# Kernel optimization log

Hardware: AMD Instinct MI355X
Metric: run time of the kernel (lower is better)

The kernel has to match this reference:

```python
import jax, jax.numpy as jnp
import numpy as np

N_EMBD = 384
HEAD_SIZE = 16

def setup_inputs() -> dict:
    key = jax.random.key(0)
    k1, k2, k3, k4 = jax.random.split(key, 4)
    B, T = 4, 4096
    x = jax.random.normal(k1, (B, T, N_EMBD), dtype=jnp.float32)
    # nn.Linear(n_embd, head_size, bias=False): y = x @ W^T, W: [head_size, n_embd].
    # Store transposed [n_embd, head_size] for direct matmul.
    s = 1.0 / np.sqrt(N_EMBD)
    Wk = jax.random.uniform(k2, (N_EMBD, HEAD_SIZE), jnp.float32, -s, s)
    Wq = jax.random.uniform(k3, (N_EMBD, HEAD_SIZE), jnp.float32, -s, s)
    Wv = jax.random.uniform(k4, (N_EMBD, HEAD_SIZE), jnp.float32, -s, s)
    return {"x": x, "Wk": Wk, "Wq": Wq, "Wv": Wv}

def reference(x, Wk, Wq, Wv):
    B, T, C = x.shape
    k = x @ Wk  # [B,T,H]
    q = x @ Wq
    v = x @ Wv
    scale = k.shape[-1] ** -0.5
    wei = jnp.einsum('bth,bsh->bts', q, k) * scale  # [B,T,T]
    causal = jnp.tril(jnp.ones((T, T), dtype=bool))
    wei = jnp.where(causal, wei, -jnp.inf)
    wei = jax.nn.softmax(wei, axis=-1)
    out = jnp.einsum('bts,bsh->bth', wei, v)  # [B,T,H]
    return out
```

## Files before the change

### kernel.cpp

```cpp
#include <hip/hip_runtime.h>


constexpr int B_DIM = 4;
constexpr int T_SEQ = 4096;
constexpr int C_DIM = 384;
constexpr int H_DIM = 16;
constexpr int NROW  = B_DIM * T_SEQ;

constexpr int WTROW = 392;
constexpr int WTMAT = 16 * WTROW;

typedef __bf16 bf16x8 __attribute__((ext_vector_type(8)));
typedef float  f32x4  __attribute__((ext_vector_type(4)));

__device__ __forceinline__ unsigned short f2bf(float f) {
  unsigned int u = __builtin_bit_cast(unsigned int, f);
  u += 0x7fffu + ((u >> 16) & 1u);
  return (unsigned short)(u >> 16);
}
__device__ __forceinline__ bf16x8 as_bf16x8(uint4 u) {
  return __builtin_bit_cast(bf16x8, u);
}
__device__ __forceinline__ unsigned cvt_pk_bf16(float lo, float hi) {
  unsigned r;
  asm("v_cvt_pk_bf16_f32 %0, %1, %2" : "=v"(r) : "v"(lo), "v"(hi));
  return r;
}

__global__ __launch_bounds__(512) void qkvw(
    const float* __restrict__ x,  const float* __restrict__ Wk,
    const float* __restrict__ Wq, const float* __restrict__ Wv,
    unsigned short* __restrict__ Kb,
    unsigned short* __restrict__ Qb,
    unsigned short* __restrict__ VTb)
{
  __shared__ __attribute__((aligned(16))) unsigned short WTl[3 * WTMAT];
  __shared__ float mrg[4][12 * 64];

  const int tid  = threadIdx.x;
  const int w    = tid >> 6;
  const int lane = tid & 63;
  const int quad = lane >> 4;
  const int col  = lane & 15;
  const int pair = w >> 1;
  const int kw   = w & 1;
  const int tile = (blockIdx.x << 2) | pair;
  const int r0   = tile << 4;
  const int kb   = kw * 6;

  {
    const float* const Ws[3] = {Wk, Wq, Wv};
#pragma unroll
    for (int e = 0; e < 9; ++e) {
      const int i4 = e * 512 + tid;
      const int m  = i4 / 1536;
      const int j4 = (i4 - m * 1536) * 4;
      const int k  = j4 >> 4;
      const int n  = j4 & 15;
      const float4 v = *reinterpret_cast<const float4*>(Ws[m] + j4);
      unsigned short* const dst = WTl + m * WTMAT + k;
      dst[(n + 0) * WTROW] = f2bf(v.x);
      dst[(n + 1) * WTROW] = f2bf(v.y);
      dst[(n + 2) * WTROW] = f2bf(v.z);
      dst[(n + 3) * WTROW] = f2bf(v.w);
    }
  }
  __syncthreads();

  const float4* __restrict__ xp =
      reinterpret_cast<const float4*>(x + (size_t)(r0 + col) * C_DIM) + quad * 2;
  float4 araw[12];
#pragma unroll
  for (int kk = 0; kk < 6; ++kk) {
    araw[2 * kk]     = xp[(kb + kk) * 8];
    araw[2 * kk + 1] = xp[(kb + kk) * 8 + 1];
  }

  const unsigned short* const bkl = WTl + col * WTROW + quad * 8;

  f32x4 ck = {0.f, 0.f, 0.f, 0.f};
  f32x4 cq = {0.f, 0.f, 0.f, 0.f};
  f32x4 cv = {0.f, 0.f, 0.f, 0.f};
#pragma unroll
  for (int kk = 0; kk < 6; ++kk) {
    uint4 pk;
    const float4 a0 = araw[2 * kk], a1 = araw[2 * kk + 1];
    pk.x = cvt_pk_bf16(a0.x, a0.y);
    pk.y = cvt_pk_bf16(a0.z, a0.w);
    pk.z = cvt_pk_bf16(a1.x, a1.y);
    pk.w = cvt_pk_bf16(a1.z, a1.w);
    const bf16x8 av = as_bf16x8(pk);
    const int ko = (kb + kk) * 32;
    const uint4 fk = *reinterpret_cast<const uint4*>(bkl + ko);
    const uint4 fq = *reinterpret_cast<const uint4*>(bkl + WTMAT + ko);
    const uint4 fv = *reinterpret_cast<const uint4*>(bkl + 2 * WTMAT + ko);
    ck = __builtin_amdgcn_mfma_f32_16x16x32_bf16(av, as_bf16x8(fk), ck, 0, 0, 0);
    cq = __builtin_amdgcn_mfma_f32_16x16x32_bf16(av, as_bf16x8(fq), cq, 0, 0, 0);
    cv = __builtin_amdgcn_mfma_f32_16x16x32_bf16(av, as_bf16x8(fv), cv, 0, 0, 0);
  }

  if (kw == 1) {
#pragma unroll
    for (int r = 0; r < 4; ++r) {
      mrg[pair][r * 64 + lane]       = ck[r];
      mrg[pair][(4 + r) * 64 + lane] = cq[r];
      mrg[pair][(8 + r) * 64 + lane] = cv[r];
    }
  }
  __syncthreads();
  if (kw == 0) {
    const float SC = 0.25f * 1.44269504088896341f;
#pragma unroll
    for (int r = 0; r < 4; ++r) {
      const float vk = ck[r] + mrg[pair][r * 64 + lane];
      const float vq = cq[r] + mrg[pair][(4 + r) * 64 + lane];
      const float vv = cv[r] + mrg[pair][(8 + r) * 64 + lane];
      const int row = r0 + quad * 4 + r;
      Kb[row * 16 + col]      = f2bf(vk);
      Qb[row * 32 + col]      = f2bf(vq * SC);
      Qb[row * 32 + 16 + col] = 0;
      const int bb = row >> 12, t = row & 4095;
      VTb[(((size_t)(bb * 16 + col)) << 12) + t] = f2bf(vv);
    }
  }
}

__global__ __launch_bounds__(512) void flash_v9(
    const unsigned short* __restrict__ Qb,
    const unsigned short* __restrict__ Kb,
    const unsigned short* __restrict__ VTb,
    float* __restrict__ out)
{
  const int tid  = threadIdx.x;
  const int w    = tid >> 6;
  const int lane = tid & 63;
  const int quad = lane >> 4;
  const int col  = lane & 15;
  const int p    = blockIdx.x >> 2;
  const int b    = blockIdx.x & 3;
  const int qtA  = 255 - p;
  const int qtB  = p;
  const int nchA = (qtA + 4) >> 2;

  __shared__ __attribute__((aligned(16))) unsigned short Pl[8][16 * 72];
  __shared__ float mO[8][2][256];
  __shared__ float mL[8][2][16];
  unsigned short* const P = Pl[w];

  const unsigned short* Kbase = Kb + ((size_t)(b * T_SEQ) << 4);
  const unsigned short* Vbase = VTb + (((size_t)(b * 16 + col)) << 12);
  const int poff = col * 72 + quad * 4;

  f32x4 o = {0.f, 0.f, 0.f, 0.f};

  const uint4* qpA = reinterpret_cast<const uint4*>(
      Qb + (((size_t)(b * T_SEQ + (qtA << 4) + col)) << 5) + quad * 8);
  const uint4* qpB = reinterpret_cast<const uint4*>(
      Qb + (((size_t)(b * T_SEQ + (qtB << 4) + col)) << 5) + quad * 8);
  const bf16x8 qaA = as_bf16x8(qpA[0]);
  const bf16x8 qaB = as_bf16x8(qpB[0]);

  auto loadK = [&](int c, uint4* k4) {
    const int kt0 = c << 2;
#pragma unroll
    for (int t = 0; t < 4; ++t)
      k4[t] = *reinterpret_cast<const uint4*>(
          Kbase + (((size_t)((kt0 + t) * 16 + col)) << 4) + quad * 8);
  };
  auto loadV = [&](int c, uint4* v2) {
    v2[0] = *reinterpret_cast<const uint4*>(Vbase + c * 64 + quad * 8);
    v2[1] = *reinterpret_cast<const uint4*>(Vbase + c * 64 + 32 + quad * 8);
  };

  auto computeP = [&](int qt, bf16x8 qa, int c, const uint4* k4, float& lref) {
    const int kt0 = c << 2;
    float lsum = 0.f;
#pragma unroll
    for (int t = 0; t < 4; ++t) {
      const int kt = kt0 + t;
      f32x4 sf;
      if (kt <= qt) {
        f32x4 z = {0.f, 0.f, 0.f, 0.f};
        sf = __builtin_amdgcn_mfma_f32_16x16x32_bf16(as_bf16x8(k4[t]), qa, z, 0, 0, 0);
        if (kt == qt) {
#pragma unroll
          for (int r = 0; r < 4; ++r)
            if (quad * 4 + r > col) sf[r] = -1e30f;
        }
      } else {
#pragma unroll
        for (int r = 0; r < 4; ++r) sf[r] = -1e30f;
      }
      const float p0 = __builtin_amdgcn_exp2f(sf[0]);
      const float p1 = __builtin_amdgcn_exp2f(sf[1]);
      const float p2 = __builtin_amdgcn_exp2f(sf[2]);
      const float p3 = __builtin_amdgcn_exp2f(sf[3]);
      lsum += (p0 + p1) + (p2 + p3);
      uint2 pr;
      pr.x = cvt_pk_bf16(p0, p1);
      pr.y = cvt_pk_bf16(p2, p3);
      *reinterpret_cast<uint2*>(P + poff + t * 16) = pr;
    }
    lref += lsum;
  };

  auto doPV = [&](const uint4* v2) {
    const uint2* pp = reinterpret_cast<const uint2*>(P + col * 72);
    const uint2 a0 = pp[quad * 2],     a1 = pp[quad * 2 + 1];
    const uint2 b0 = pp[8 + quad * 2], b1 = pp[8 + quad * 2 + 1];
    const uint4 p0 = {a0.x, a0.y, a1.x, a1.y};
    const uint4 p1 = {b0.x, b0.y, b1.x, b1.y};
    o = __builtin_amdgcn_mfma_f32_16x16x32_bf16(as_bf16x8(p0), as_bf16x8(v2[0]), o, 0, 0, 0);
    o = __builtin_amdgcn_mfma_f32_16x16x32_bf16(as_bf16x8(p1), as_bf16x8(v2[1]), o, 0, 0, 0);
  };

  auto writePartial = [&](int ph, float lsum) {
    float l = lsum;
    l += __shfl_xor(l, 16);
    l += __shfl_xor(l, 32);
#pragma unroll
    for (int r = 0; r < 4; ++r)
      mO[w][ph][(quad * 4 + r) * 16 + col] = o[r];
    if (quad == 0) mL[w][ph][col] = l;
  };

  float lA = 0.f, lB = 0.f;
  uint4 k4[4], vcur[2], vnxt[2];

  int g = w;
  loadK(g, k4);
  loadV(g, vcur);
  computeP(qtA, qaA, g, k4, lA);

  int prevg = g;
  g += 8;
  while (g < 65) {
    const int c = (g < nchA) ? g : g - nchA;
    loadK(c, k4);
    loadV(c, vnxt);
    doPV(vcur);
    asm volatile("" ::: "memory");
    if (prevg < nchA && g >= nchA) {
      writePartial(0, lA);
      o = (f32x4){0.f, 0.f, 0.f, 0.f};
    }
    if (g < nchA) computeP(qtA, qaA, c, k4, lA);
    else          computeP(qtB, qaB, c, k4, lB);
    vcur[0] = vnxt[0];
    vcur[1] = vnxt[1];
    prevg = g;
    g += 8;
  }
  doPV(vcur);
  if (prevg < nchA) {
    writePartial(0, lA);
    o = (f32x4){0.f, 0.f, 0.f, 0.f};
    writePartial(1, 0.f);
  } else {
    writePartial(1, lB);
  }

  __syncthreads();

  {
    const int ph = tid >> 8;
    const int i  = tid & 255;
    float O = 0.f, L = 0.f;
#pragma unroll
    for (int ww = 0; ww < 8; ++ww) {
      O += mO[ww][ph][i];
      L += mL[ww][ph][i >> 4];
    }
    const int qt = ph ? qtB : qtA;
    out[(size_t)(b * T_SEQ + (qt << 4)) * 16 + i] = O / L;
  }
}

extern "C" void kernel_launch(void* const* d_in, const int* in_sizes, int n_in,
                              void* d_out, int out_size, void* d_ws, size_t ws_size,
                              hipStream_t stream) {
  const float* x  = (const float*)d_in[0];
  const float* Wk = (const float*)d_in[1];
  const float* Wq = (const float*)d_in[2];
  const float* Wv = (const float*)d_in[3];
  float* outp = (float*)d_out;

  unsigned short* Qb  = (unsigned short*)d_ws;
  unsigned short* Kb  = Qb + (size_t)NROW * 32;
  unsigned short* VTb = Kb + (size_t)NROW * 16 + 64;

  qkvw<<<256, 512, 0, stream>>>(x, Wk, Wq, Wv, Kb, Qb, VTb);
  flash_v9<<<512, 512, 0, stream>>>(Qb, Kb, VTb, outp);
}
```

Measured before the change: 90.16 us.

## Double flash block to 1024 threads and alias merge buffers onto P scratch

Each flash block now runs 16 waves instead of 8, so each wave handles every 16th key chunk and per-wave serial work is halved. Partial outputs are kept in registers until the end and then written into a shared slab that reuses the P scratch memory, with an extra barrier before the final reduction. The aim is more latency hiding and shorter per-block critical paths, at the cost of higher register pressure under the 1024-thread launch bound and a 16-way reduction step.

```diff
diff --git a/kernel.cpp b/kernel.cpp
--- a/kernel.cpp
+++ b/kernel.cpp
@@ -125,7 +125,7 @@
   }
 }
 
-__global__ __launch_bounds__(512) void flash_v9(
+__global__ __launch_bounds__(1024) void flash_v10(
     const unsigned short* __restrict__ Qb,
     const unsigned short* __restrict__ Kb,
     const unsigned short* __restrict__ VTb,
@@ -142,16 +142,17 @@
   const int qtB  = p;
   const int nchA = (qtA + 4) >> 2;
 
-  __shared__ __attribute__((aligned(16))) unsigned short Pl[8][16 * 72];
-  __shared__ float mO[8][2][256];
-  __shared__ float mL[8][2][16];
-  unsigned short* const P = Pl[w];
+  __shared__ __attribute__((aligned(16))) unsigned char smem[38912];
+  unsigned short* const P = (unsigned short*)smem + w * (16 * 72);
+  float* const slabO = (float*)smem;
+  float* const slabL = (float*)(smem + 36864);
 
   const unsigned short* Kbase = Kb + ((size_t)(b * T_SEQ) << 4);
   const unsigned short* Vbase = VTb + (((size_t)(b * 16 + col)) << 12);
   const int poff = col * 72 + quad * 4;
 
-  f32x4 o = {0.f, 0.f, 0.f, 0.f};
+  f32x4 o   = {0.f, 0.f, 0.f, 0.f};
+  f32x4 oSv = {0.f, 0.f, 0.f, 0.f};
 
   const uint4* qpA = reinterpret_cast<const uint4*>(
       Qb + (((size_t)(b * T_SEQ + (qtA << 4) + col)) << 5) + quad * 8);
@@ -214,16 +215,6 @@
     o = __builtin_amdgcn_mfma_f32_16x16x32_bf16(as_bf16x8(p1), as_bf16x8(v2[1]), o, 0, 0, 0);
   };
 
-  auto writePartial = [&](int ph, float lsum) {
-    float l = lsum;
-    l += __shfl_xor(l, 16);
-    l += __shfl_xor(l, 32);
-#pragma unroll
-    for (int r = 0; r < 4; ++r)
-      mO[w][ph][(quad * 4 + r) * 16 + col] = o[r];
-    if (quad == 0) mL[w][ph][col] = l;
-  };
-
   float lA = 0.f, lB = 0.f;
   uint4 k4[4], vcur[2], vnxt[2];
 
@@ -233,7 +224,7 @@
   computeP(qtA, qaA, g, k4, lA);
 
   int prevg = g;
-  g += 8;
+  g += 16;
   while (g < 65) {
     const int c = (g < nchA) ? g : g - nchA;
     loadK(c, k4);
@@ -241,7 +232,7 @@
     doPV(vcur);
     asm volatile("" ::: "memory");
     if (prevg < nchA && g >= nchA) {
-      writePartial(0, lA);
+      oSv = o;
       o = (f32x4){0.f, 0.f, 0.f, 0.f};
     }
     if (g < nchA) computeP(qtA, qaA, c, k4, lA);
@@ -249,27 +240,46 @@
     vcur[0] = vnxt[0];
     vcur[1] = vnxt[1];
     prevg = g;
-    g += 8;
+    g += 16;
   }
   doPV(vcur);
+
+  f32x4 oA, oB;
   if (prevg < nchA) {
-    writePartial(0, lA);
-    o = (f32x4){0.f, 0.f, 0.f, 0.f};
-    writePartial(1, 0.f);
+    oA = o;
+    oB = (f32x4){0.f, 0.f, 0.f, 0.f};
   } else {
-    writePartial(1, lB);
-  }
+    oA = oSv;
+    oB = o;
+  }
+
+  lA += __shfl_xor(lA, 16);
+  lA += __shfl_xor(lA, 32);
+  lB += __shfl_xor(lB, 16);
+  lB += __shfl_xor(lB, 32);
 
   __syncthreads();
 
-  {
+#pragma unroll
+  for (int r = 0; r < 4; ++r) {
+    slabO[(w * 2 + 0) * 256 + (quad * 4 + r) * 16 + col] = oA[r];
+    slabO[(w * 2 + 1) * 256 + (quad * 4 + r) * 16 + col] = oB[r];
+  }
+  if (quad == 0) {
+    slabL[(w * 2 + 0) * 16 + col] = lA;
+    slabL[(w * 2 + 1) * 16 + col] = lB;
+  }
+
+  __syncthreads();
+
+  if (tid < 512) {
     const int ph = tid >> 8;
     const int i  = tid & 255;
     float O = 0.f, L = 0.f;
 #pragma unroll
-    for (int ww = 0; ww < 8; ++ww) {
-      O += mO[ww][ph][i];
-      L += mL[ww][ph][i >> 4];
+    for (int ww = 0; ww < 16; ++ww) {
+      O += slabO[(ww * 2 + ph) * 256 + i];
+      L += slabL[(ww * 2 + ph) * 16 + (i >> 4)];
     }
     const int qt = ph ? qtB : qtA;
     out[(size_t)(b * T_SEQ + (qt << 4)) * 16 + i] = O / L;
@@ -290,5 +300,5 @@
   unsigned short* VTb = Kb + (size_t)NROW * 16 + 64;
 
   qkvw<<<256, 512, 0, stream>>>(x, Wk, Wq, Wv, Kb, Qb, VTb);
-  flash_v9<<<512, 512, 0, stream>>>(Qb, Kb, VTb, outp);
-}
+  flash_v10<<<512, 1024, 0, stream>>>(Qb, Kb, VTb, outp);
+}
```

After: 94.02 us. +4.3%, slower.
